# Performance work log

Hardware: AMD Instinct MI355X
Metric: run time of the kernel (lower is better)

## Reference

```python
import jax, jax.numpy as jnp
import numpy as np

B, H, S, DK = 2, 16, 2048, 64

def setup_inputs() -> dict:
    key = jax.random.key(0)
    kq, kk, kv = jax.random.split(key, 3)
    shape = (B, H, S, DK)
    return {
        "multi_head_q": jax.random.normal(kq, shape, dtype=jnp.float32),
        "multi_head_k": jax.random.normal(kk, shape, dtype=jnp.float32),
        "multi_head_v": jax.random.normal(kv, shape, dtype=jnp.float32),
    }

def reference(multi_head_q, multi_head_k, multi_head_v):
    d_k = multi_head_q.shape[-1]
    scale = 1.0 / jnp.sqrt(jnp.asarray(d_k, dtype=multi_head_q.dtype))
    # scores: [B, H, S, S]
    scores = jnp.einsum("bhqd,bhkd->bhqk", multi_head_q, multi_head_k) * scale
    attn = jax.nn.softmax(scores, axis=-1)
    # z: [B, H, S, DK]
    z = jnp.einsum("bhqk,bhkd->bhqd", attn, multi_head_v)
    # transpose heads to [B, S, H, DK] then merge -> [B, S, H*DK]
    b, h, s, d = z.shape
    return jnp.swapaxes(z, 1, 2).reshape(b, s, h * d)
```

## Files before the change

kernel.cpp:

```cpp
#include <hip/hip_runtime.h>
#include <cmath>


#define S_LEN   2048
#define D_HEAD  64
#define NHEADS  16
#define TQ      128
#define TK      64
#define LDSTR   72

typedef short bfrag8 __attribute__((ext_vector_type(8)));
typedef float f32x4  __attribute__((ext_vector_type(4)));
typedef int   i32x2  __attribute__((ext_vector_type(2)));
typedef int   i32x4  __attribute__((ext_vector_type(4)));

static __device__ __forceinline__ short f2bf(float f) {
  unsigned int u = __builtin_bit_cast(unsigned int, f);
  u = (u + 0x7fffu + ((u >> 16) & 1u)) >> 16;
  return (short)(unsigned short)u;
}

static __device__ __forceinline__ int pk2bf(float a, float b) {
#if __has_builtin(__builtin_amdgcn_cvt_pk_bf16_f32)
  typedef __bf16 bf16x2 __attribute__((ext_vector_type(2)));
  bf16x2 r = __builtin_amdgcn_cvt_pk_bf16_f32(a, b);
  return __builtin_bit_cast(int, r);
#else
  return (int)(unsigned short)f2bf(a) | ((int)(unsigned short)f2bf(b) << 16);
#endif
}

static __device__ __forceinline__ float fexp2(float x) {
#if __has_builtin(__builtin_amdgcn_exp2f)
  return __builtin_amdgcn_exp2f(x);
#else
  return exp2f(x);
#endif
}

__global__ __launch_bounds__(256, 2)
void fa_fwd(const float* __restrict__ Q, const float* __restrict__ K,
            const float* __restrict__ V, float* __restrict__ Out) {
  __shared__ short Ks [TK     * LDSTR];
  __shared__ short VsT[D_HEAD * LDSTR];
  __shared__ short Ps [TQ     * LDSTR];

  const int tid  = threadIdx.x;
  const int wid  = tid >> 6;
  const int lane = tid & 63;
  const int quad = lane >> 4;
  const int r    = lane & 15;
  const int qb   = 32 * wid;

  const int bh = blockIdx.y;
  const int q0 = blockIdx.x * TQ;

  const float* Qg = Q + (size_t)bh * S_LEN * D_HEAD;
  const float* Kg = K + (size_t)bh * S_LEN * D_HEAD;
  const float* Vg = V + (size_t)bh * S_LEN * D_HEAD;

  const float qscale = 0.125f * 1.44269504088896340736f;

  bfrag8 qf[2][2];
#pragma unroll
  for (int nt = 0; nt < 2; ++nt) {
#pragma unroll
    for (int ks = 0; ks < 2; ++ks) {
      const float* qp = Qg + (size_t)(q0 + qb + 16 * nt + r) * D_HEAD + 32 * ks + 8 * quad;
      float4 a = *(const float4*)qp;
      float4 b = *(const float4*)(qp + 4);
      i32x4 w;
      w[0] = pk2bf(a.x * qscale, a.y * qscale);
      w[1] = pk2bf(a.z * qscale, a.w * qscale);
      w[2] = pk2bf(b.x * qscale, b.y * qscale);
      w[3] = pk2bf(b.z * qscale, b.w * qscale);
      qf[nt][ks] = __builtin_bit_cast(bfrag8, w);
    }
  }

  float4 kpre[4];
  float  vpre[16];

  auto load_tile = [&](int k0) {
#pragma unroll
    for (int i = 0; i < 4; ++i) {
      int e = (i * 256 + tid) * 4;
      int row = e >> 6, col = e & 63;
      kpre[i] = *(const float4*)(Kg + (size_t)(k0 + row) * D_HEAD + col);
    }
    const float* vp = Vg + (size_t)(k0 + wid * 16) * D_HEAD + lane;
#pragma unroll
    for (int j = 0; j < 16; ++j) vpre[j] = vp[(size_t)j * D_HEAD];
  };

  auto store_tile = [&]() {
#pragma unroll
    for (int i = 0; i < 4; ++i) {
      int e = (i * 256 + tid) * 4;
      int row = e >> 6, col = e & 63;
      i32x2 w;
      w[0] = pk2bf(kpre[i].x, kpre[i].y);
      w[1] = pk2bf(kpre[i].z, kpre[i].w);
      *(i32x2*)&Ks[row * LDSTR + col] = w;
    }
    i32x4 w0, w1;
#pragma unroll
    for (int j = 0; j < 4; ++j) w0[j] = pk2bf(vpre[2 * j],     vpre[2 * j + 1]);
#pragma unroll
    for (int j = 0; j < 4; ++j) w1[j] = pk2bf(vpre[8 + 2 * j], vpre[9 + 2 * j]);
    *(i32x4*)&VsT[lane * LDSTR + wid * 16]     = w0;
    *(i32x4*)&VsT[lane * LDSTR + wid * 16 + 8] = w1;
  };

  f32x4 acc[4][2];
#pragma unroll
  for (int mt = 0; mt < 4; ++mt)
#pragma unroll
    for (int nt = 0; nt < 2; ++nt)
      acc[mt][nt] = (f32x4){0.f, 0.f, 0.f, 0.f};

  float lrun[2] = {0.f, 0.f};

  load_tile(0);

  for (int k0 = 0; k0 < S_LEN; k0 += TK) {
    __syncthreads();

    store_tile();
    if (k0 + TK < S_LEN) load_tile(k0 + TK);

    __syncthreads();

    f32x4 st[4][2];
#pragma unroll
    for (int mt = 0; mt < 4; ++mt)
#pragma unroll
      for (int nt = 0; nt < 2; ++nt)
        st[mt][nt] = (f32x4){0.f, 0.f, 0.f, 0.f};

#pragma unroll
    for (int ks = 0; ks < 2; ++ks) {
      bfrag8 af[4];
#pragma unroll
      for (int mt = 0; mt < 4; ++mt)
        af[mt] = *(const bfrag8*)&Ks[(r + 16 * mt) * LDSTR + quad * 8 + 32 * ks];
#pragma unroll
      for (int mt = 0; mt < 4; ++mt)
#pragma unroll
        for (int nt = 0; nt < 2; ++nt)
          st[mt][nt] = __builtin_amdgcn_mfma_f32_16x16x32_bf16(af[mt], qf[nt][ks], st[mt][nt], 0, 0, 0);
    }

#pragma unroll
    for (int nt = 0; nt < 2; ++nt) {
      float ssum = 0.f;
#pragma unroll
      for (int mt = 0; mt < 4; ++mt) {
        float p0 = fexp2(st[mt][nt][0]);
        float p1 = fexp2(st[mt][nt][1]);
        float p2 = fexp2(st[mt][nt][2]);
        float p3 = fexp2(st[mt][nt][3]);
        ssum += (p0 + p1) + (p2 + p3);
        i32x2 w;
        w[0] = pk2bf(p0, p1);
        w[1] = pk2bf(p2, p3);
        *(i32x2*)&Ps[(qb + 16 * nt + r) * LDSTR + 16 * mt + 4 * quad] = w;
      }
      lrun[nt] += ssum;
    }

#pragma unroll
    for (int ks = 0; ks < 2; ++ks) {
      bfrag8 av[4], bp[2];
#pragma unroll
      for (int mt = 0; mt < 4; ++mt)
        av[mt] = *(const bfrag8*)&VsT[(r + 16 * mt) * LDSTR + quad * 8 + 32 * ks];
#pragma unroll
      for (int nt = 0; nt < 2; ++nt)
        bp[nt] = *(const bfrag8*)&Ps[(qb + 16 * nt + r) * LDSTR + quad * 8 + 32 * ks];
#pragma unroll
      for (int mt = 0; mt < 4; ++mt)
#pragma unroll
        for (int nt = 0; nt < 2; ++nt)
          acc[mt][nt] = __builtin_amdgcn_mfma_f32_16x16x32_bf16(av[mt], bp[nt], acc[mt][nt], 0, 0, 0);
    }
  }

  const int bb = bh >> 4, hh = bh & 15;
#pragma unroll
  for (int nt = 0; nt < 2; ++nt) {
    float l = lrun[nt];
    l += __shfl_xor(l, 16);
    l += __shfl_xor(l, 32);
    float inv = 1.0f / l;
    int qg = q0 + qb + 16 * nt + r;
    float* op = Out + ((size_t)bb * S_LEN + qg) * (NHEADS * D_HEAD) + hh * D_HEAD;
#pragma unroll
    for (int mt = 0; mt < 4; ++mt) {
      float4 o;
      o.x = acc[mt][nt][0] * inv; o.y = acc[mt][nt][1] * inv;
      o.z = acc[mt][nt][2] * inv; o.w = acc[mt][nt][3] * inv;
      *(float4*)(op + 16 * mt + 4 * quad) = o;
    }
  }
}

extern "C" void kernel_launch(void* const* d_in, const int* in_sizes, int n_in,
                              void* d_out, int out_size, void* d_ws, size_t ws_size,
                              hipStream_t stream) {
  const float* Q = (const float*)d_in[0];
  const float* K = (const float*)d_in[1];
  const float* V = (const float*)d_in[2];
  float* O = (float*)d_out;
  dim3 grid(S_LEN / TQ, 2 * NHEADS);
  fa_fwd<<<grid, 256, 0, stream>>>(Q, K, V, O);
}
```

Before: 149.4 us.

## Double-buffer K/V LDS tiles to overlap staging with compute

K and V LDS tiles become two ping-pong buffers, and the loop is unrolled by two. The next tile's bf16 conversion and LDS store now happen right after computing on the current buffer. This halves the block-wide barriers per key tile and lets stores overlap other waves' MFMA work. In exchange, LDS use per block rises, which may limit occupancy at two blocks per CU, and the unrolled lambda body grows code size and register pressure.

```diff
diff --git a/kernel.cpp b/kernel.cpp
--- a/kernel.cpp
+++ b/kernel.cpp
@@ -7,6 +7,7 @@
 #define NHEADS  16
 #define TQ      128
 #define TK      64
+#define NITER   (S_LEN / TK)
 #define LDSTR   72
 
 typedef short bfrag8 __attribute__((ext_vector_type(8)));
@@ -41,9 +42,9 @@
 __global__ __launch_bounds__(256, 2)
 void fa_fwd(const float* __restrict__ Q, const float* __restrict__ K,
             const float* __restrict__ V, float* __restrict__ Out) {
-  __shared__ short Ks [TK     * LDSTR];
-  __shared__ short VsT[D_HEAD * LDSTR];
-  __shared__ short Ps [TQ     * LDSTR];
+  __shared__ short Ks [2][TK     * LDSTR];
+  __shared__ short VsT[2][D_HEAD * LDSTR];
+  __shared__ short Ps [TQ * LDSTR];
 
   const int tid  = threadIdx.x;
   const int wid  = tid >> 6;
@@ -93,7 +94,7 @@
     for (int j = 0; j < 16; ++j) vpre[j] = vp[(size_t)j * D_HEAD];
   };
 
-  auto store_tile = [&]() {
+  auto store_tile = [&](short* ksb, short* vsb) {
 #pragma unroll
     for (int i = 0; i < 4; ++i) {
       int e = (i * 256 + tid) * 4;
@@ -101,15 +102,15 @@
       i32x2 w;
       w[0] = pk2bf(kpre[i].x, kpre[i].y);
       w[1] = pk2bf(kpre[i].z, kpre[i].w);
-      *(i32x2*)&Ks[row * LDSTR + col] = w;
+      *(i32x2*)&ksb[row * LDSTR + col] = w;
     }
     i32x4 w0, w1;
 #pragma unroll
     for (int j = 0; j < 4; ++j) w0[j] = pk2bf(vpre[2 * j],     vpre[2 * j + 1]);
 #pragma unroll
     for (int j = 0; j < 4; ++j) w1[j] = pk2bf(vpre[8 + 2 * j], vpre[9 + 2 * j]);
-    *(i32x4*)&VsT[lane * LDSTR + wid * 16]     = w0;
-    *(i32x4*)&VsT[lane * LDSTR + wid * 16 + 8] = w1;
+    *(i32x4*)&vsb[lane * LDSTR + wid * 16]     = w0;
+    *(i32x4*)&vsb[lane * LDSTR + wid * 16 + 8] = w1;
   };
 
   f32x4 acc[4][2];
@@ -121,16 +122,7 @@
 
   float lrun[2] = {0.f, 0.f};
 
-  load_tile(0);
-
-  for (int k0 = 0; k0 < S_LEN; k0 += TK) {
-    __syncthreads();
-
-    store_tile();
-    if (k0 + TK < S_LEN) load_tile(k0 + TK);
-
-    __syncthreads();
-
+  auto compute = [&](const short* ksb, const short* vsb) {
     f32x4 st[4][2];
 #pragma unroll
     for (int mt = 0; mt < 4; ++mt)
@@ -143,7 +135,7 @@
       bfrag8 af[4];
 #pragma unroll
       for (int mt = 0; mt < 4; ++mt)
-        af[mt] = *(const bfrag8*)&Ks[(r + 16 * mt) * LDSTR + quad * 8 + 32 * ks];
+        af[mt] = *(const bfrag8*)&ksb[(r + 16 * mt) * LDSTR + quad * 8 + 32 * ks];
 #pragma unroll
       for (int mt = 0; mt < 4; ++mt)
 #pragma unroll
@@ -174,7 +166,7 @@
       bfrag8 av[4], bp[2];
 #pragma unroll
       for (int mt = 0; mt < 4; ++mt)
-        av[mt] = *(const bfrag8*)&VsT[(r + 16 * mt) * LDSTR + quad * 8 + 32 * ks];
+        av[mt] = *(const bfrag8*)&vsb[(r + 16 * mt) * LDSTR + quad * 8 + 32 * ks];
 #pragma unroll
       for (int nt = 0; nt < 2; ++nt)
         bp[nt] = *(const bfrag8*)&Ps[(qb + 16 * nt + r) * LDSTR + quad * 8 + 32 * ks];
@@ -183,6 +175,24 @@
 #pragma unroll
         for (int nt = 0; nt < 2; ++nt)
           acc[mt][nt] = __builtin_amdgcn_mfma_f32_16x16x32_bf16(av[mt], bp[nt], acc[mt][nt], 0, 0, 0);
+    }
+  };
+
+  load_tile(0);
+  store_tile(Ks[0], VsT[0]);
+  load_tile(TK);
+
+  for (int it = 0; it < NITER; it += 2) {
+    __syncthreads();
+    compute(Ks[0], VsT[0]);
+    store_tile(Ks[1], VsT[1]);
+    if (it + 2 < NITER) load_tile((it + 2) * TK);
+
+    __syncthreads();
+    compute(Ks[1], VsT[1]);
+    if (it + 2 < NITER) {
+      store_tile(Ks[0], VsT[0]);
+      if (it + 3 < NITER) load_tile((it + 3) * TK);
     }
   }
 
```

After: 146.7 us. About the same (-1.8%).
